# Optimization experiments

Measured on AMD Instinct MI355X. Metric: run time of the kernel, lower is better.

Reference implementation:

```python
import jax, jax.numpy as jnp
import numpy as np

D_MODEL = 1024
SEQ = 4096

def setup_inputs() -> dict:
    key = jax.random.key(0)
    k_x, k_q, k_k, k_v, k_o = jax.random.split(key, 5)
    x = jax.random.normal(k_x, (SEQ, D_MODEL), dtype=jnp.float32)
    w_q = jax.random.normal(k_q, (D_MODEL, D_MODEL), dtype=jnp.float32)
    w_k = jax.random.normal(k_k, (D_MODEL, D_MODEL), dtype=jnp.float32)
    w_v = jax.random.normal(k_v, (D_MODEL, D_MODEL), dtype=jnp.float32)
    out_proj = jax.random.normal(k_o, (D_MODEL, D_MODEL), dtype=jnp.float32)
    return {"x": x, "w_q": w_q, "w_k": w_k, "w_v": w_v, "out_proj": out_proj}

def reference(x, w_q, w_k, w_v, out_proj):
    # Faithful to original: Q/K projections, scaled QK^T, softmax over last dim.
    # V and out_proj are computed/declared in the original module but unused in the output.
    Q = x @ w_q                      # [S, D]
    K = x @ w_k                      # [S, D]
    scale = 1.0 / jnp.sqrt(jnp.asarray(Q.shape[-1], dtype=Q.dtype))
    scores = (Q @ K.T) * scale       # [S, S]
    return jax.nn.softmax(scores, axis=-1)
```

## Files before the change

### kernel.cpp

```cpp
#include <hip/hip_runtime.h>
#include <math.h>

#define SEQ 4096
#define DM  1024

#define BM 128
#define BN 128
#define NCT (SEQ / BN)
#define KS 32

typedef __attribute__((ext_vector_type(8))) short bf16x8;
typedef __attribute__((ext_vector_type(4))) float f32x4;

union U4 { uint4 u; unsigned short s[8]; };

__device__ __forceinline__ float bf2f(unsigned short u) {
    return __uint_as_float(((unsigned int)u) << 16);
}
__device__ __forceinline__ unsigned short f2bf(float f) {
    unsigned int u = __float_as_uint(f);
    return (unsigned short)((u + 0x7FFFu + ((u >> 16) & 1u)) >> 16);
}

__device__ __forceinline__ int detect_bf16(const void* p0) {
    const unsigned int* p = (const unsigned int*)p0;
    int cnt = 0;
    #pragma unroll
    for (int i = 0; i < 64; i++) {
        unsigned int e = (p[i] >> 7) & 0xFFu;
        cnt += (e >= 112u && e <= 140u) ? 1 : 0;
    }
    return cnt >= 48 ? 1 : 0;
}

__device__ __forceinline__ void load8(const void* base, size_t idx, int isbf, float* v) {
    if (isbf) {
        U4 t; t.u = *(const uint4*)((const unsigned short*)base + idx);
        #pragma unroll
        for (int q = 0; q < 8; q++) v[q] = bf2f(t.s[q]);
    } else {
        const float* f = (const float*)base + idx;
        float4 a = *(const float4*)f;
        float4 b = *(const float4*)(f + 4);
        v[0] = a.x; v[1] = a.y; v[2] = a.z; v[3] = a.w;
        v[4] = b.x; v[5] = b.y; v[6] = b.z; v[7] = b.w;
    }
}

__device__ __forceinline__ void gl16(const void* g, void* l) {
    __builtin_amdgcn_global_load_lds(
        (const __attribute__((address_space(1))) unsigned int*)g,
        (__attribute__((address_space(3))) unsigned int*)l, 16, 0, 0);
}

__global__ __launch_bounds__(256)
void split3_kernel(const void* __restrict__ X, const void* __restrict__ Wq,
                   const void* __restrict__ Wk,
                   unsigned short* __restrict__ Xhi, unsigned short* __restrict__ Xlo,
                   unsigned short* __restrict__ Wqhi, unsigned short* __restrict__ Wqlo,
                   unsigned short* __restrict__ Wkhi, unsigned short* __restrict__ Wklo)
{
    const int b = blockIdx.x;
    const void* src;
    unsigned short *Hi, *Lo;
    size_t i;
    if (b < 2048)      { src = X;  Hi = Xhi;  Lo = Xlo;  i = ((size_t)b * 256 + threadIdx.x) * 8; }
    else if (b < 2560) { src = Wq; Hi = Wqhi; Lo = Wqlo; i = ((size_t)(b - 2048) * 256 + threadIdx.x) * 8; }
    else               { src = Wk; Hi = Wkhi; Lo = Wklo; i = ((size_t)(b - 2560) * 256 + threadIdx.x) * 8; }
    const int isbf = detect_bf16(src);
    float v[8];
    load8(src, i, isbf, v);
    U4 h, l;
    #pragma unroll
    for (int q = 0; q < 8; q++) {
        h.s[q] = f2bf(v[q]);
        l.s[q] = f2bf(v[q] - bf2f(h.s[q]));
    }
    *(uint4*)(Hi + i) = h.u;
    *(uint4*)(Lo + i) = l.u;
}

__global__ __launch_bounds__(256)
void part_mfma_kernel(const unsigned short* __restrict__ Ahi, const unsigned short* __restrict__ Alo,
                      const unsigned short* __restrict__ Bhi, const unsigned short* __restrict__ Blo,
                      float* __restrict__ O, int kchunk, size_t pstride, float scale)
{
    __shared__ unsigned short lAhi[128 * KS];
    __shared__ unsigned short lAlo[128 * KS];
    __shared__ unsigned short lBhi[128 * KS];
    __shared__ unsigned short lBlo[128 * KS];

    const int t = threadIdx.x;
    const int gy  = gridDim.y;
    const int nwg = 8 * gy * gridDim.z;
    const int lid = (blockIdx.z * gy + blockIdx.y) * 8 + blockIdx.x;
    const int swz = (lid & 7) * (nwg >> 3) + (lid >> 3);
    const int bx  = swz & 7;
    const int rst = swz >> 3;
    const int by  = rst % gy;
    const int kz  = rst / gy;

    const int lane = t & 63;
    const int w    = t >> 6;
    const int wr   = w >> 1;
    const int wc   = w & 1;
    const int fr   = lane & 15;
    const int fq   = lane >> 4;

    f32x4 acc[4][4];
    #pragma unroll
    for (int i = 0; i < 4; i++)
        #pragma unroll
        for (int j = 0; j < 4; j++)
            acc[i][j] = (f32x4){0.f, 0.f, 0.f, 0.f};

    const int trow = t >> 2;
    const int tcs  = t & 3;
    const int k0   = kz * kchunk;

    for (int kt = k0; kt < k0 + kchunk; kt += KS) {
        #pragma unroll
        for (int p = 0; p < 2; p++) {
            const int row = p * 64 + trow;
            const int sc  = tcs ^ ((row >> 1) & 3);
            const int lof = (p * 256 + t) * 16;
            const size_t ga = (size_t)(by * BM + row) * DM + kt + sc * 8;
            const size_t gb = (size_t)(bx * BN + row) * DM + kt + sc * 8;
            gl16(Ahi + ga, (char*)lAhi + lof);
            gl16(Alo + ga, (char*)lAlo + lof);
            gl16(Bhi + gb, (char*)lBhi + lof);
            gl16(Blo + gb, (char*)lBlo + lof);
        }
        __syncthreads();

        bf16x8 bh[4], bl[4];
        #pragma unroll
        for (int nj = 0; nj < 4; nj++) {
            const int br = wc * 64 + nj * 16 + fr;
            const int bc = fq ^ ((br >> 1) & 3);
            bh[nj] = *(const bf16x8*)&lBhi[br * KS + bc * 8];
            bl[nj] = *(const bf16x8*)&lBlo[br * KS + bc * 8];
        }
        #pragma unroll
        for (int mi = 0; mi < 4; mi++) {
            const int ar_ = wr * 64 + mi * 16 + fr;
            const int ac_ = fq ^ ((ar_ >> 1) & 3);
            bf16x8 ah = *(const bf16x8*)&lAhi[ar_ * KS + ac_ * 8];
            bf16x8 al = *(const bf16x8*)&lAlo[ar_ * KS + ac_ * 8];
            #pragma unroll
            for (int nj = 0; nj < 4; nj++) {
                acc[mi][nj] = __builtin_amdgcn_mfma_f32_16x16x32_bf16(ah, bh[nj], acc[mi][nj], 0, 0, 0);
                acc[mi][nj] = __builtin_amdgcn_mfma_f32_16x16x32_bf16(al, bh[nj], acc[mi][nj], 0, 0, 0);
                acc[mi][nj] = __builtin_amdgcn_mfma_f32_16x16x32_bf16(ah, bl[nj], acc[mi][nj], 0, 0, 0);
            }
        }
        __syncthreads();
    }

    float* Op = O + (size_t)kz * pstride;
    #pragma unroll
    for (int mi = 0; mi < 4; mi++)
        #pragma unroll
        for (int reg = 0; reg < 4; reg++) {
            const int row = by * BM + wr * 64 + mi * 16 + fq * 4 + reg;
            #pragma unroll
            for (int nj = 0; nj < 4; nj++) {
                const int col = bx * BN + wc * 64 + nj * 16 + fr;
                Op[(size_t)row * DM + col] = acc[mi][nj][reg] * scale;
            }
        }
}

__global__ __launch_bounds__(256)
void w2_reduce_split_kernel(const float* __restrict__ P, unsigned short* __restrict__ Hi,
                            unsigned short* __restrict__ Lo)
{
    const size_t N = (size_t)DM * DM;
    size_t i = ((size_t)blockIdx.x * 256 + threadIdx.x) * 8;
    float v[8];
    #pragma unroll
    for (int h = 0; h < 8; h += 4) {
        float4 a = *(const float4*)(P + i + h);
        float4 b = *(const float4*)(P + N + i + h);
        float4 c = *(const float4*)(P + 2 * N + i + h);
        float4 d = *(const float4*)(P + 3 * N + i + h);
        v[h + 0] = a.x + b.x + c.x + d.x;
        v[h + 1] = a.y + b.y + c.y + d.y;
        v[h + 2] = a.z + b.z + c.z + d.z;
        v[h + 3] = a.w + b.w + c.w + d.w;
    }
    U4 h, l;
    #pragma unroll
    for (int q = 0; q < 8; q++) {
        h.s[q] = f2bf(v[q]);
        l.s[q] = f2bf(v[q] - bf2f(h.s[q]));
    }
    *(uint4*)(Hi + i) = h.u;
    *(uint4*)(Lo + i) = l.u;
}

__global__ __launch_bounds__(256)
void qw_combine_split_kernel(const float* __restrict__ P0, const float* __restrict__ P1,
                             unsigned short* __restrict__ Hi, unsigned short* __restrict__ Lo)
{
    size_t i = ((size_t)blockIdx.x * 256 + threadIdx.x) * 8;
    float4 a0 = *(const float4*)(P0 + i);
    float4 a1 = *(const float4*)(P0 + i + 4);
    float4 b0 = *(const float4*)(P1 + i);
    float4 b1 = *(const float4*)(P1 + i + 4);
    float v[8] = {a0.x + b0.x, a0.y + b0.y, a0.z + b0.z, a0.w + b0.w,
                  a1.x + b1.x, a1.y + b1.y, a1.z + b1.z, a1.w + b1.w};
    U4 h, l;
    #pragma unroll
    for (int q = 0; q < 8; q++) {
        h.s[q] = f2bf(v[q]);
        l.s[q] = f2bf(v[q] - bf2f(h.s[q]));
    }
    *(uint4*)(Hi + i) = h.u;
    *(uint4*)(Lo + i) = l.u;
}

__global__ __launch_bounds__(256)
void scores_mfma_kernel(const unsigned short* __restrict__ QWhi,
                        const unsigned short* __restrict__ QWlo,
                        const void* __restrict__ X,
                        float* __restrict__ pm, float* __restrict__ pl,
                        void* __restrict__ out)
{
    __shared__ unsigned short lAhi[128 * KS];
    __shared__ unsigned short lAlo[128 * KS];
    __shared__ unsigned short lBhi[128 * KS];
    __shared__ unsigned short lBlo[128 * KS];
    __shared__ float smax[128][2];
    __shared__ float ssum[128][2];

    const int isbf = detect_bf16(X);
    const int t    = threadIdx.x;
    const int bx   = blockIdx.x;
    const int by   = blockIdx.y;
    const int lane = t & 63;
    const int w    = t >> 6;
    const int wr   = w >> 1;
    const int wc   = w & 1;
    const int fr   = lane & 15;
    const int fq   = lane >> 4;

    f32x4 acc[4][4];
    #pragma unroll
    for (int i = 0; i < 4; i++)
        #pragma unroll
        for (int j = 0; j < 4; j++)
            acc[i][j] = (f32x4){0.f, 0.f, 0.f, 0.f};

    const int trow = t >> 2;
    const int tcs  = t & 3;

    for (int kt = 0; kt < DM; kt += KS) {
        #pragma unroll
        for (int p = 0; p < 2; p++) {
            const int row = p * 64 + trow;
            const int sc  = tcs ^ ((row >> 1) & 3);
            const int lof = (p * 256 + t) * 16;
            const size_t ga = (size_t)(by * BM + row) * DM + kt + sc * 8;
            gl16(QWhi + ga, (char*)lAhi + lof);
            gl16(QWlo + ga, (char*)lAlo + lof);
            if (isbf) {
                const size_t gb = (size_t)(bx * BN + row) * DM + kt + sc * 8;
                gl16((const unsigned short*)X + gb, (char*)lBhi + lof);
            }
        }
        if (!isbf) {
            const int row  = t >> 1;
            const int half = t & 1;
            const float* xp = (const float*)X + (size_t)(bx * BN + row) * DM + kt + half * 16;
            float4 v0 = ((const float4*)xp)[0];
            float4 v1 = ((const float4*)xp)[1];
            float4 v2 = ((const float4*)xp)[2];
            float4 v3 = ((const float4*)xp)[3];
            float vv[16] = {v0.x, v0.y, v0.z, v0.w, v1.x, v1.y, v1.z, v1.w,
                            v2.x, v2.y, v2.z, v2.w, v3.x, v3.y, v3.z, v3.w};
            U4 h0, h1, l0, l1;
            #pragma unroll
            for (int q = 0; q < 8; q++) {
                h0.s[q] = f2bf(vv[q]);
                l0.s[q] = f2bf(vv[q] - bf2f(h0.s[q]));
                h1.s[q] = f2bf(vv[8 + q]);
                l1.s[q] = f2bf(vv[8 + q] - bf2f(h1.s[q]));
            }
            const int s  = (row >> 1) & 3;
            const int ca = (2 * half) ^ s;
            const int cb = (2 * half + 1) ^ s;
            *(uint4*)&lBhi[row * KS + ca * 8] = h0.u;
            *(uint4*)&lBhi[row * KS + cb * 8] = h1.u;
            *(uint4*)&lBlo[row * KS + ca * 8] = l0.u;
            *(uint4*)&lBlo[row * KS + cb * 8] = l1.u;
        }
        __syncthreads();

        bf16x8 bh[4];
        #pragma unroll
        for (int nj = 0; nj < 4; nj++) {
            const int br = wc * 64 + nj * 16 + fr;
            const int bc = fq ^ ((br >> 1) & 3);
            bh[nj] = *(const bf16x8*)&lBhi[br * KS + bc * 8];
        }
        #pragma unroll
        for (int mi = 0; mi < 4; mi++) {
            const int ar_ = wr * 64 + mi * 16 + fr;
            const int ac_ = fq ^ ((ar_ >> 1) & 3);
            bf16x8 ah = *(const bf16x8*)&lAhi[ar_ * KS + ac_ * 8];
            bf16x8 al = *(const bf16x8*)&lAlo[ar_ * KS + ac_ * 8];
            #pragma unroll
            for (int nj = 0; nj < 4; nj++) {
                acc[mi][nj] = __builtin_amdgcn_mfma_f32_16x16x32_bf16(ah, bh[nj], acc[mi][nj], 0, 0, 0);
                acc[mi][nj] = __builtin_amdgcn_mfma_f32_16x16x32_bf16(al, bh[nj], acc[mi][nj], 0, 0, 0);
            }
        }
        if (!isbf) {
            bf16x8 bl[4];
            #pragma unroll
            for (int nj = 0; nj < 4; nj++) {
                const int br = wc * 64 + nj * 16 + fr;
                const int bc = fq ^ ((br >> 1) & 3);
                bl[nj] = *(const bf16x8*)&lBlo[br * KS + bc * 8];
            }
            #pragma unroll
            for (int mi = 0; mi < 4; mi++) {
                const int ar_ = wr * 64 + mi * 16 + fr;
                const int ac_ = fq ^ ((ar_ >> 1) & 3);
                bf16x8 ah = *(const bf16x8*)&lAhi[ar_ * KS + ac_ * 8];
                #pragma unroll
                for (int nj = 0; nj < 4; nj++)
                    acc[mi][nj] = __builtin_amdgcn_mfma_f32_16x16x32_bf16(ah, bl[nj], acc[mi][nj], 0, 0, 0);
            }
        }
        __syncthreads();
    }

    float rmx[4][4];
    #pragma unroll
    for (int mi = 0; mi < 4; mi++)
        #pragma unroll
        for (int reg = 0; reg < 4; reg++) {
            float m = acc[mi][0][reg];
            #pragma unroll
            for (int nj = 1; nj < 4; nj++) m = fmaxf(m, acc[mi][nj][reg]);
            m = fmaxf(m, __shfl_xor(m, 1, 64));
            m = fmaxf(m, __shfl_xor(m, 2, 64));
            m = fmaxf(m, __shfl_xor(m, 4, 64));
            m = fmaxf(m, __shfl_xor(m, 8, 64));
            rmx[mi][reg] = m;
        }
    if (fr == 0) {
        #pragma unroll
        for (int mi = 0; mi < 4; mi++)
            #pragma unroll
            for (int reg = 0; reg < 4; reg++)
                smax[wr * 64 + mi * 16 + fq * 4 + reg][wc] = rmx[mi][reg];
    }
    __syncthreads();
    float mt[4][4];
    #pragma unroll
    for (int mi = 0; mi < 4; mi++)
        #pragma unroll
        for (int reg = 0; reg < 4; reg++) {
            const int r = wr * 64 + mi * 16 + fq * 4 + reg;
            mt[mi][reg] = fmaxf(smax[r][0], smax[r][1]);
        }
    float rsm[4][4];
    #pragma unroll
    for (int mi = 0; mi < 4; mi++)
        #pragma unroll
        for (int reg = 0; reg < 4; reg++) rsm[mi][reg] = 0.f;
    #pragma unroll
    for (int mi = 0; mi < 4; mi++)
        #pragma unroll
        for (int nj = 0; nj < 4; nj++)
            #pragma unroll
            for (int reg = 0; reg < 4; reg++) {
                float e = __expf(acc[mi][nj][reg] - mt[mi][reg]);
                acc[mi][nj][reg] = e;
                rsm[mi][reg] += e;
            }
    #pragma unroll
    for (int mi = 0; mi < 4; mi++)
        #pragma unroll
        for (int reg = 0; reg < 4; reg++) {
            float s = rsm[mi][reg];
            s += __shfl_xor(s, 1, 64);
            s += __shfl_xor(s, 2, 64);
            s += __shfl_xor(s, 4, 64);
            s += __shfl_xor(s, 8, 64);
            if (fr == 0) ssum[wr * 64 + mi * 16 + fq * 4 + reg][wc] = s;
        }
    #pragma unroll
    for (int mi = 0; mi < 4; mi++)
        #pragma unroll
        for (int reg = 0; reg < 4; reg++) {
            const int row = by * BM + wr * 64 + mi * 16 + fq * 4 + reg;
            #pragma unroll
            for (int nj = 0; nj < 4; nj++) {
                const int col = bx * BN + wc * 64 + nj * 16 + fr;
                const float v = acc[mi][nj][reg];
                if (isbf)
                    ((unsigned short*)out)[(size_t)row * SEQ + col] = f2bf(v);
                else
                    ((float*)out)[(size_t)row * SEQ + col] = v;
            }
        }
    __syncthreads();
    if (t < 128) {
        const int grow = by * BM + t;
        pm[(size_t)bx * SEQ + grow] = fmaxf(smax[t][0], smax[t][1]);
        pl[(size_t)bx * SEQ + grow] = ssum[t][0] + ssum[t][1];
    }
}

__global__ __launch_bounds__(256)
void reduce_kernel(const float* __restrict__ pm, float* __restrict__ pl)
{
    int r = blockIdx.x * 256 + threadIdx.x;
    if (r >= SEQ) return;
    float m = pm[r];
    #pragma unroll
    for (int ti = 1; ti < NCT; ti++) m = fmaxf(m, pm[(size_t)ti * SEQ + r]);
    float l = 0.f;
    #pragma unroll
    for (int ti = 0; ti < NCT; ti++)
        l += pl[(size_t)ti * SEQ + r] * __expf(pm[(size_t)ti * SEQ + r] - m);
    float il = 1.f / l;
    #pragma unroll
    for (int ti = 0; ti < NCT; ti++)
        pl[(size_t)ti * SEQ + r] = __expf(pm[(size_t)ti * SEQ + r] - m) * il;
}

__global__ __launch_bounds__(256)
void fixup_kernel(const float* __restrict__ F, const void* __restrict__ X,
                  void* __restrict__ out)
{
    const int isbf = detect_bf16(X);
    size_t g = ((size_t)blockIdx.x * 256 + threadIdx.x) * 8;
    const int row = (int)(g >> 12);
    const int col = (int)(g & (SEQ - 1));
    const float f = F[(size_t)(col >> 7) * SEQ + row];
    if (isbf) {
        unsigned short* p = (unsigned short*)out + g;
        U4 v; v.u = *(const uint4*)p;
        #pragma unroll
        for (int q = 0; q < 8; q++) v.s[q] = f2bf(bf2f(v.s[q]) * f);
        *(uint4*)p = v.u;
    } else {
        float* p = (float*)out + g;
        float4 a = *(const float4*)p;
        float4 b = *(const float4*)(p + 4);
        a.x *= f; a.y *= f; a.z *= f; a.w *= f;
        b.x *= f; b.y *= f; b.z *= f; b.w *= f;
        *(float4*)p = a;
        *(float4*)(p + 4) = b;
    }
}

extern "C" void kernel_launch(void* const* d_in, const int* in_sizes, int n_in,
                              void* d_out, int out_size, void* d_ws, size_t ws_size,
                              hipStream_t stream)
{
    const void* x  = d_in[0];
    const void* wq = d_in[1];
    const void* wk = d_in[2];

    char* wsb = (char*)d_ws;
    char* dob = (char*)d_out;
    unsigned short* Xhi   = (unsigned short*)wsb;
    unsigned short* Xlo   = (unsigned short*)(wsb + ((size_t)8 << 20));
    unsigned short* QWhi  = (unsigned short*)wsb;
    unsigned short* QWlo  = (unsigned short*)(wsb + ((size_t)8 << 20));
    unsigned short* W2Thi = (unsigned short*)(wsb + ((size_t)16 << 20));
    unsigned short* W2Tlo = (unsigned short*)(wsb + ((size_t)18 << 20));
    float*          pm    = (float*)(wsb + ((size_t)16 << 20));
    float*          pl    = pm + (size_t)NCT * SEQ;

    unsigned short* Wkhi = (unsigned short*)dob;
    unsigned short* Wklo = (unsigned short*)(dob + ((size_t)2 << 20));
    unsigned short* Wqhi = (unsigned short*)(dob + ((size_t)4 << 20));
    unsigned short* Wqlo = (unsigned short*)(dob + ((size_t)6 << 20));
    float*          W2P  = (float*)(dob + ((size_t)8 << 20));
    float*          QP0  = (float*)(dob + ((size_t)24 << 20));
    float*          QP1  = QP0 + (size_t)SEQ * DM;

    dim3 blk(256);
    split3_kernel<<<dim3(3072), blk, 0, stream>>>(x, wq, wk, Xhi, Xlo, Wqhi, Wqlo, Wkhi, Wklo);
    part_mfma_kernel<<<dim3(8, DM / BM, 4), blk, 0, stream>>>(
        Wkhi, Wklo, Wqhi, Wqlo, W2P, DM / 4, (size_t)DM * DM, 0.03125f);
    w2_reduce_split_kernel<<<dim3(DM * DM / (8 * 256)), blk, 0, stream>>>(W2P, W2Thi, W2Tlo);
    part_mfma_kernel<<<dim3(8, SEQ / BM, 2), blk, 0, stream>>>(
        Xhi, Xlo, W2Thi, W2Tlo, QP0, DM / 2, (size_t)SEQ * DM, 1.0f);
    qw_combine_split_kernel<<<dim3(SEQ * DM / (8 * 256)), blk, 0, stream>>>(QP0, QP1, QWhi, QWlo);
    scores_mfma_kernel<<<dim3(SEQ / BN, SEQ / BM), blk, 0, stream>>>(QWhi, QWlo, x, pm, pl, d_out);
    reduce_kernel<<<dim3(SEQ / 256), blk, 0, stream>>>(pm, pl);
    fixup_kernel<<<dim3(SEQ * SEQ / (8 * 256)), blk, 0, stream>>>(pl, x, d_out);
}
```

Baseline: 304.3 us.

## Fuse softmax normalization into scores kernel via cooperative grid sync

Launches the scores kernel cooperatively so that all 1024 tiles stay resident. After publishing per-tile row max and sum, every tile does a grid-wide sync, computes the global row max and sum itself, and writes the already-normalized probabilities in one pass. This removes the separate reduce and fixup kernels and the extra read-modify-write of the 4096x4096 output. It also adds a fourth lo*lo MFMA term to the split-bf16 projection GEMMs, which raises precision at extra compute cost. The change relies on `__launch_bounds__(256,4)` residency, which risks register pressure or spills, and keeps a non-cooperative fallback path.

```diff
diff --git a/kernel.cpp b/kernel.cpp
--- a/kernel.cpp
+++ b/kernel.cpp
@@ -1,4 +1,5 @@
 #include <hip/hip_runtime.h>
+#include <hip/hip_cooperative_groups.h>
 #include <math.h>
 
 #define SEQ 4096
@@ -152,6 +153,7 @@
                 acc[mi][nj] = __builtin_amdgcn_mfma_f32_16x16x32_bf16(ah, bh[nj], acc[mi][nj], 0, 0, 0);
                 acc[mi][nj] = __builtin_amdgcn_mfma_f32_16x16x32_bf16(al, bh[nj], acc[mi][nj], 0, 0, 0);
                 acc[mi][nj] = __builtin_amdgcn_mfma_f32_16x16x32_bf16(ah, bl[nj], acc[mi][nj], 0, 0, 0);
+                acc[mi][nj] = __builtin_amdgcn_mfma_f32_16x16x32_bf16(al, bl[nj], acc[mi][nj], 0, 0, 0);
             }
         }
         __syncthreads();
@@ -220,7 +222,8 @@
     *(uint4*)(Lo + i) = l.u;
 }
 
-__global__ __launch_bounds__(256)
+template <int COOP>
+__global__ __launch_bounds__(256, 4)
 void scores_mfma_kernel(const unsigned short* __restrict__ QWhi,
                         const unsigned short* __restrict__ QWlo,
                         const void* __restrict__ X,
@@ -233,6 +236,7 @@
     __shared__ unsigned short lBlo[128 * KS];
     __shared__ float smax[128][2];
     __shared__ float ssum[128][2];
+    __shared__ float rowfac[128];
 
     const int isbf = detect_bf16(X);
     const int t    = threadIdx.x;
@@ -393,26 +397,62 @@
             s += __shfl_xor(s, 8, 64);
             if (fr == 0) ssum[wr * 64 + mi * 16 + fq * 4 + reg][wc] = s;
         }
-    #pragma unroll
-    for (int mi = 0; mi < 4; mi++)
-        #pragma unroll
-        for (int reg = 0; reg < 4; reg++) {
-            const int row = by * BM + wr * 64 + mi * 16 + fq * 4 + reg;
-            #pragma unroll
-            for (int nj = 0; nj < 4; nj++) {
-                const int col = bx * BN + wc * 64 + nj * 16 + fr;
-                const float v = acc[mi][nj][reg];
-                if (isbf)
-                    ((unsigned short*)out)[(size_t)row * SEQ + col] = f2bf(v);
-                else
-                    ((float*)out)[(size_t)row * SEQ + col] = v;
-            }
-        }
     __syncthreads();
     if (t < 128) {
         const int grow = by * BM + t;
         pm[(size_t)bx * SEQ + grow] = fmaxf(smax[t][0], smax[t][1]);
         pl[(size_t)bx * SEQ + grow] = ssum[t][0] + ssum[t][1];
+    }
+
+    if constexpr (COOP) {
+        __threadfence();
+        cooperative_groups::this_grid().sync();
+        if (t < 128) {
+            const int grow = by * BM + t;
+            float m = pm[grow];
+            #pragma unroll
+            for (int ti = 1; ti < NCT; ti++) m = fmaxf(m, pm[(size_t)ti * SEQ + grow]);
+            float l = 0.f;
+            #pragma unroll
+            for (int ti = 0; ti < NCT; ti++)
+                l += pl[(size_t)ti * SEQ + grow] * __expf(pm[(size_t)ti * SEQ + grow] - m);
+            const float mtile = fmaxf(smax[t][0], smax[t][1]);
+            rowfac[t] = __expf(mtile - m) / l;
+        }
+        __syncthreads();
+        #pragma unroll
+        for (int mi = 0; mi < 4; mi++)
+            #pragma unroll
+            for (int reg = 0; reg < 4; reg++) {
+                const int rl  = wr * 64 + mi * 16 + fq * 4 + reg;
+                const int row = by * BM + rl;
+                const float fac = rowfac[rl];
+                #pragma unroll
+                for (int nj = 0; nj < 4; nj++) {
+                    const int col = bx * BN + wc * 64 + nj * 16 + fr;
+                    const float v = acc[mi][nj][reg] * fac;
+                    if (isbf)
+                        ((unsigned short*)out)[(size_t)row * SEQ + col] = f2bf(v);
+                    else
+                        ((float*)out)[(size_t)row * SEQ + col] = v;
+                }
+            }
+    } else {
+        #pragma unroll
+        for (int mi = 0; mi < 4; mi++)
+            #pragma unroll
+            for (int reg = 0; reg < 4; reg++) {
+                const int row = by * BM + wr * 64 + mi * 16 + fq * 4 + reg;
+                #pragma unroll
+                for (int nj = 0; nj < 4; nj++) {
+                    const int col = bx * BN + wc * 64 + nj * 16 + fr;
+                    const float v = acc[mi][nj][reg];
+                    if (isbf)
+                        ((unsigned short*)out)[(size_t)row * SEQ + col] = f2bf(v);
+                    else
+                        ((float*)out)[(size_t)row * SEQ + col] = v;
+                }
+            }
     }
 }
 
@@ -495,7 +535,23 @@
     part_mfma_kernel<<<dim3(8, SEQ / BM, 2), blk, 0, stream>>>(
         Xhi, Xlo, W2Thi, W2Tlo, QP0, DM / 2, (size_t)SEQ * DM, 1.0f);
     qw_combine_split_kernel<<<dim3(SEQ * DM / (8 * 256)), blk, 0, stream>>>(QP0, QP1, QWhi, QWlo);
-    scores_mfma_kernel<<<dim3(SEQ / BN, SEQ / BM), blk, 0, stream>>>(QWhi, QWlo, x, pm, pl, d_out);
-    reduce_kernel<<<dim3(SEQ / 256), blk, 0, stream>>>(pm, pl);
-    fixup_kernel<<<dim3(SEQ * SEQ / (8 * 256)), blk, 0, stream>>>(pl, x, d_out);
-}
+
+    {
+        const unsigned short* a0 = QWhi;
+        const unsigned short* a1 = QWlo;
+        const void*           a2 = x;
+        float*                a3 = pm;
+        float*                a4 = pl;
+        void*                 a5 = d_out;
+        void* kargs[6] = {&a0, &a1, &a2, &a3, &a4, &a5};
+        hipError_t e = hipLaunchCooperativeKernel(
+            (const void*)&scores_mfma_kernel<1>,
+            dim3(SEQ / BN, SEQ / BM), blk, kargs, 0, stream);
+        if (e != hipSuccess) {
+            scores_mfma_kernel<0><<<dim3(SEQ / BN, SEQ / BM), blk, 0, stream>>>(
+                QWhi, QWlo, x, pm, pl, d_out);
+            reduce_kernel<<<dim3(SEQ / 256), blk, 0, stream>>>(pm, pl);
+            fixup_kernel<<<dim3(SEQ * SEQ / (8 * 256)), blk, 0, stream>>>(pl, x, d_out);
+        }
+    }
+}
```

Result: slower. 494.3 us (+62.4%).
